# Kernel optimization log

Hardware: AMD Instinct MI355X
Metric: run time of the kernel (lower is better)

Reference implementation:

```python
import jax, jax.numpy as jnp
import numpy as np

N_NODES, N_GRAPHS, N_EDGES = 40960, 1024, 163840


def setup_inputs() -> dict:
    key = jax.random.key(0)
    ks = jax.random.split(key, 40)
    w = lambda k, s: jax.random.normal(k, s, jnp.float32) * 0.05
    inp = {
        "x": jax.random.normal(ks[0], (N_NODES, 78), jnp.float32),
        "edge_index": jax.random.randint(ks[1], (2, N_EDGES), 0, N_NODES, jnp.int32),
        "batch": jnp.repeat(jnp.arange(N_GRAPHS, dtype=jnp.int32), N_NODES // N_GRAPHS),
        "target1": jax.random.normal(ks[2], (N_GRAPHS, 750, 20), jnp.float32),
        "target2": jax.random.randint(ks[3], (N_GRAPHS, 750), 0, 26, jnp.int32),
        # GCN layers
        "W1": w(ks[4], (78, 78)), "b1": jnp.zeros((78,), jnp.float32),
        "W2": w(ks[5], (78, 156)), "b2": jnp.zeros((156,), jnp.float32),
        "W3": w(ks[6], (156, 312)), "b3": jnp.zeros((312,), jnp.float32),
        "Wg1": w(ks[7], (312, 1024)), "bg1": jnp.zeros((1024,), jnp.float32),
        "Wg2": w(ks[8], (1024, 128)), "bg2": jnp.zeros((128,), jnp.float32),
        # protein branch
        "emb": w(ks[9], (26, 128)),
        "Wc2": w(ks[10], (32, 750, 8)), "bc2": jnp.zeros((32,), jnp.float32),
        "Wxt2": w(ks[11], (32 * 121, 128)), "bxt2": jnp.zeros((128,), jnp.float32),
        "Wc1": w(ks[12], (32, 750, 8)), "bc1": jnp.zeros((32,), jnp.float32),
        "Wxt1": w(ks[13], (416, 128)), "bxt1": jnp.zeros((128,), jnp.float32),
        # fusion head
        "Wf1": w(ks[14], (384, 1024)), "bf1": jnp.zeros((1024,), jnp.float32),
        "Wf2": w(ks[15], (1024, 512)), "bf2": jnp.zeros((512,), jnp.float32),
        "Wo": w(ks[16], (512, 1)), "bo": jnp.zeros((1,), jnp.float32),
    }
    return inp


def _conv1d(x, w, b):
    # x: [B, C_in, L], w: [C_out, C_in, K] -> [B, C_out, L-K+1]
    y = jax.lax.conv_general_dilated(x, w, (1,), "VALID",
                                     dimension_numbers=("NCH", "OIH", "NCH"))
    return y + b[None, :, None]


def reference(x, edge_index, batch, target1, target2,
              W1, b1, W2, b2, W3, b3, Wg1, bg1, Wg2, bg2,
              emb, Wc2, bc2, Wxt2, bxt2, Wc1, bc1, Wxt1, bxt1,
              Wf1, bf1, Wf2, bf2, Wo, bo):
    N = x.shape[0]
    loop = jnp.arange(N, dtype=edge_index.dtype)
    src = jnp.concatenate([edge_index[0], loop])  # message source j
    dst = jnp.concatenate([edge_index[1], loop])  # aggregation target i
    # symmetric GCN normalization with self-loops (degree from dst, as in PyG)
    deg = jnp.zeros((N,), x.dtype).at[dst].add(1.0)
    dinv = jax.lax.rsqrt(deg)  # deg >= 1 due to self loops
    norm = (dinv[src] * dinv[dst])[:, None]

    def gcn(h, W, b):
        m = (h @ W)[src] * norm
        return jax.ops.segment_sum(m, dst, num_segments=N) + b

    h = jax.nn.relu(gcn(x, W1, b1))
    h = jax.nn.relu(gcn(h, W2, b2))
    h = jax.nn.relu(gcn(h, W3, b3))
    # global max pool per graph
    g = jax.ops.segment_max(h, batch, num_segments=N_GRAPHS)
    g = jax.nn.relu(g @ Wg1 + bg1)
    g = g @ Wg2 + bg2  # dropout is identity at inference

    # protein branch 2: embedding -> conv1d over channels=750
    e = emb[target2]                         # [B, 750, 128]
    xt2 = _conv1d(e, Wc2, bc2)               # [B, 32, 121]
    xt2 = xt2.reshape(-1, 32 * 121) @ Wxt2 + bxt2

    # protein branch 1: raw float features
    xt1 = _conv1d(target1, Wc1, bc1)         # [B, 32, 13]
    xt1 = xt1.reshape(-1, 416) @ Wxt1 + bxt1

    xc = jnp.concatenate([g, xt1, xt2], axis=1)  # [B, 384]
    xc = jax.nn.relu(xc @ Wf1 + bf1)
    xc = jax.nn.relu(xc @ Wf2 + bf2)
    return xc @ Wo + bo
```

## Files before the change

kernel.cpp:

```cpp
#include <hip/hip_runtime.h>
#include <hip/hip_bf16.h>

#define NN 40960
#define NE 163840
#define NB 1024

typedef __attribute__((ext_vector_type(8))) short short8;
typedef __attribute__((ext_vector_type(4))) float floatx4;

__device__ inline unsigned short f2bf(float f) {
    union { float f; unsigned u; } v; v.f = f;
    unsigned r = v.u + 0x7fffu + ((v.u >> 16) & 1u);
    return (unsigned short)(r >> 16);
}
__device__ inline float bf2f(unsigned short s) {
    union { unsigned u; float f; } v; v.u = ((unsigned)s) << 16; return v.f;
}
__device__ inline unsigned pack2bf(float lo, float hi) {
    return (unsigned)f2bf(lo) | ((unsigned)f2bf(hi) << 16);
}

static const size_t o_dinv = 0, o_g312 = 40960, o_g1024 = 360448, o_xc = 1409024,
                    o_f1 = 1802240, o_f2 = 2850816, o_b1v = 3375104, o_b2v = 3375232,
                    o_iws = 3375360, o_bufA = 3621124, o_bufB = 16400644;

__global__ void k_hist(const int* __restrict__ dst, int* __restrict__ cnt) {
    int e = blockIdx.x * 256 + threadIdx.x;
    if (e < NE) atomicAdd(&cnt[dst[e]], 1);
}

__global__ __launch_bounds__(1024) void k_scan1(const int* __restrict__ cnt, int* __restrict__ offTmp,
                                                int* __restrict__ blockSum, float* __restrict__ dinv) {
    __shared__ int lds[1024];
    int tid = threadIdx.x;
    int i = blockIdx.x * 1024 + tid;
    int v = cnt[i];
    dinv[i] = rsqrtf((float)v + 1.0f);
    lds[tid] = v;
    __syncthreads();
    for (int s = 1; s < 1024; s <<= 1) {
        int t = (tid >= s) ? lds[tid - s] : 0;
        __syncthreads();
        lds[tid] += t;
        __syncthreads();
    }
    offTmp[i] = lds[tid] - v;
    if (tid == 1023) blockSum[blockIdx.x] = lds[1023];
}

__global__ __launch_bounds__(64) void k_scan2(const int* __restrict__ blockSum, int* __restrict__ blockOff) {
    int l = threadIdx.x;
    int s = (l < 40) ? blockSum[l] : 0;
    int orig = s;
    for (int d = 1; d < 64; d <<= 1) {
        int t = __shfl_up(s, d);
        if (l >= d) s += t;
    }
    if (l < 40) blockOff[l] = s - orig;
}

__global__ __launch_bounds__(1024) void k_scan3(int* __restrict__ off, int* __restrict__ cur,
                                                const int* __restrict__ blockOff) {
    int i = blockIdx.x * 1024 + threadIdx.x;
    int o = off[i] + blockOff[blockIdx.x];
    off[i] = o;
    cur[i] = o;
    if (i == NN - 1) off[NN] = NE;
}

__global__ void k_fill(const int* __restrict__ ei, int* __restrict__ cur, int* __restrict__ srcOut) {
    int e = blockIdx.x * 256 + threadIdx.x;
    if (e >= NE) return;
    int s = ei[e], d = ei[NE + e];
    int pos = atomicAdd(&cur[d], 1);
    srcOut[pos] = s;
}

__global__ __launch_bounds__(256) void k_cvt_wt(const float* __restrict__ W1, const float* __restrict__ W2,
                                                const float* __restrict__ W3, const float* __restrict__ Wg1,
                                                const float* __restrict__ Wg2, const float* __restrict__ Wf1,
                                                const float* __restrict__ Wf2, unsigned short* __restrict__ dst) {
    const int cum[8]  = {0, 128, 320, 640, 1664, 1792, 2816, 3328};
    const int KP[7]   = {96, 96, 160, 320, 1024, 384, 1024};
    const int KB[7]   = {78, 78, 156, 312, 1024, 384, 1024};
    const int NNm[7]  = {78, 156, 312, 1024, 128, 1024, 512};
    const size_t OFF[7] = {0, 12288, 30720, 81920, 409600, 540672, 933888};
    int m = 0;
    int bx = blockIdx.x;
    while (m < 6 && bx >= cum[m + 1]) m++;
    int r = bx - cum[m];
    const float* src = (m == 0) ? W1 : (m == 1) ? W2 : (m == 2) ? W3 : (m == 3) ? Wg1
                     : (m == 4) ? Wg2 : (m == 5) ? Wf1 : Wf2;
    int kp = KP[m], kb = KB[m], nn = NNm[m];
    unsigned short* d = dst + OFF[m] + (size_t)r * kp;
    for (int k = threadIdx.x; k < kp; k += 256) {
        float v = (r < nn && k < kb) ? src[(size_t)k * nn + r] : 0.f;
        d[k] = f2bf(v);
    }
}

__global__ __launch_bounds__(64) void k_agg_x(const float* __restrict__ x, const float* __restrict__ dinv,
                                              const int* __restrict__ off, const int* __restrict__ srcs,
                                              unsigned* __restrict__ out) {
    int n = blockIdx.x;
    int f = threadIdx.x;
    if (f >= 48) return;
    if (f >= 39) { out[(size_t)n * 48 + f] = 0; return; }
    float di = dinv[n];
    float2 sv = *(const float2*)&x[(size_t)n * 78 + 2 * f];
    float a0 = sv.x * di * di, a1 = sv.y * di * di;
    int e0 = off[n], e1 = off[n + 1];
    int e = e0;
    for (; e + 4 <= e1; e += 4) {
        int s0 = srcs[e], s1 = srcs[e + 1], s2 = srcs[e + 2], s3 = srcs[e + 3];
        float d0 = dinv[s0] * di, d1 = dinv[s1] * di, d2 = dinv[s2] * di, d3 = dinv[s3] * di;
        float2 v0 = *(const float2*)&x[(size_t)s0 * 78 + 2 * f];
        float2 v1 = *(const float2*)&x[(size_t)s1 * 78 + 2 * f];
        float2 v2 = *(const float2*)&x[(size_t)s2 * 78 + 2 * f];
        float2 v3 = *(const float2*)&x[(size_t)s3 * 78 + 2 * f];
        a0 += v0.x * d0 + v1.x * d1 + v2.x * d2 + v3.x * d3;
        a1 += v0.y * d0 + v1.y * d1 + v2.y * d2 + v3.y * d3;
    }
    for (; e < e1; e++) {
        int s = srcs[e];
        float dd = dinv[s] * di;
        float2 v = *(const float2*)&x[(size_t)s * 78 + 2 * f];
        a0 += v.x * dd; a1 += v.y * dd;
    }
    out[(size_t)n * 48 + f] = pack2bf(a0, a1);
}

__global__ void k_agg16(const unsigned* __restrict__ h, const float* __restrict__ dinv,
                        const int* __restrict__ off, const int* __restrict__ srcs,
                        unsigned* __restrict__ out, int F2) {
    int n = blockIdx.x;
    int f = threadIdx.x;
    if (f >= F2) return;
    float di = dinv[n];
    unsigned s0v = h[(size_t)n * F2 + f];
    float a0 = bf2f((unsigned short)(s0v & 0xffff)) * di * di;
    float a1 = bf2f((unsigned short)(s0v >> 16)) * di * di;
    int e0 = off[n], e1 = off[n + 1];
    int e = e0;
    for (; e + 4 <= e1; e += 4) {
        int s0 = srcs[e], s1 = srcs[e + 1], s2 = srcs[e + 2], s3 = srcs[e + 3];
        float d0 = dinv[s0] * di, d1 = dinv[s1] * di, d2 = dinv[s2] * di, d3 = dinv[s3] * di;
        unsigned v0 = h[(size_t)s0 * F2 + f];
        unsigned v1 = h[(size_t)s1 * F2 + f];
        unsigned v2 = h[(size_t)s2 * F2 + f];
        unsigned v3 = h[(size_t)s3 * F2 + f];
        a0 += bf2f((unsigned short)(v0 & 0xffff)) * d0 + bf2f((unsigned short)(v1 & 0xffff)) * d1
            + bf2f((unsigned short)(v2 & 0xffff)) * d2 + bf2f((unsigned short)(v3 & 0xffff)) * d3;
        a1 += bf2f((unsigned short)(v0 >> 16)) * d0 + bf2f((unsigned short)(v1 >> 16)) * d1
            + bf2f((unsigned short)(v2 >> 16)) * d2 + bf2f((unsigned short)(v3 >> 16)) * d3;
    }
    for (; e < e1; e++) {
        int s = srcs[e];
        float dd = dinv[s] * di;
        unsigned v = h[(size_t)s * F2 + f];
        a0 += bf2f((unsigned short)(v & 0xffff)) * dd;
        a1 += bf2f((unsigned short)(v >> 16)) * dd;
    }
    out[(size_t)n * F2 + f] = pack2bf(a0, a1);
}

__global__ void k_segmax16(const unsigned short* __restrict__ h, unsigned short* __restrict__ g) {
    int gr = blockIdx.x, f = threadIdx.x;
    if (f >= 320) return;
    if (f >= 312) { g[(size_t)gr * 320 + f] = 0; return; }
    float m = 0.0f;
    const unsigned short* base = h + (size_t)gr * 40 * 312 + f;
    for (int i = 0; i < 40; i++) m = fmaxf(m, bf2f(base[(size_t)i * 312]));
    g[(size_t)gr * 320 + f] = f2bf(m);
}

#define LDST 72
template <bool ABF16, bool OUTBF16, bool ATOMIC, bool RELU_OUT>
__global__ __launch_bounds__(256) void gemm_bt(const void* __restrict__ Av, const unsigned short* __restrict__ Bt,
                                               const float* __restrict__ bias, void* __restrict__ Cv,
                                               int Nn, int Npad, int Kpad, int Klim,
                                               int lda, int ldb, int ldc, int ksplit) {
    __shared__ __align__(16) unsigned short As[64 * LDST];
    __shared__ __align__(16) unsigned short Bs[64 * LDST];
    const float* Af = (const float*)Av;
    const unsigned short* A16 = (const unsigned short*)Av;
    float* Cf = (float*)Cv;
    unsigned short* C16 = (unsigned short*)Cv;
    int bn0 = blockIdx.x * 64;
    int bm0 = blockIdx.y * 64;
    int k0 = blockIdx.z * ksplit;
    int kend = k0 + ksplit; if (kend > Kpad) kend = Kpad;
    int tid = threadIdx.x;
    int w = tid >> 6, l = tid & 63, q = l >> 4, r = l & 15;
    int wr = w >> 1, wc = w & 1;

    floatx4 acc[2][2];
#pragma unroll
    for (int i = 0; i < 2; i++)
#pragma unroll
        for (int c = 0; c < 2; c++) acc[i][c] = (floatx4)0.0f;

    int mA = tid >> 2, kcA = (tid & 3) * 8;
    int nB = tid >> 2, kcB = (tid & 3) * 8;
    int gmA = bm0 + mA;
    int gnB = bn0 + nB;

    for (int kt = k0; kt < kend; kt += 32) {
        if (ABF16) {
            *(short8*)&As[mA * LDST + kcA] = *(const short8*)(A16 + (size_t)gmA * lda + kt + kcA);
        } else {
            const float* Ap = Af + (size_t)gmA * lda + kt + kcA;
            float av[8];
            if (kt + kcA + 8 <= Klim) {
#pragma unroll
                for (int j = 0; j < 4; j++) {
                    float2 p = *(const float2*)(Ap + j * 2);
                    av[j * 2] = p.x; av[j * 2 + 1] = p.y;
                }
            } else {
#pragma unroll
                for (int j = 0; j < 8; j++) av[j] = (kt + kcA + j < Klim) ? Ap[j] : 0.f;
            }
            short8 sv;
#pragma unroll
            for (int j = 0; j < 8; j++) sv[j] = (short)f2bf(av[j]);
            *(short8*)&As[mA * LDST + kcA] = sv;
        }
        *(short8*)&Bs[nB * LDST + kcB] = *(const short8*)(Bt + (size_t)gnB * ldb + kt + kcB);
        __syncthreads();
        short8 a0 = *(const short8*)&As[(wr * 32 + r) * LDST + q * 8];
        short8 a1 = *(const short8*)&As[(wr * 32 + 16 + r) * LDST + q * 8];
        short8 b0 = *(const short8*)&Bs[(wc * 32 + r) * LDST + q * 8];
        short8 b1 = *(const short8*)&Bs[(wc * 32 + 16 + r) * LDST + q * 8];
        acc[0][0] = __builtin_amdgcn_mfma_f32_16x16x32_bf16(a0, b0, acc[0][0], 0, 0, 0);
        acc[0][1] = __builtin_amdgcn_mfma_f32_16x16x32_bf16(a0, b1, acc[0][1], 0, 0, 0);
        acc[1][0] = __builtin_amdgcn_mfma_f32_16x16x32_bf16(a1, b0, acc[1][0], 0, 0, 0);
        acc[1][1] = __builtin_amdgcn_mfma_f32_16x16x32_bf16(a1, b1, acc[1][1], 0, 0, 0);
        __syncthreads();
    }

#pragma unroll
    for (int c2 = 0; c2 < 2; c2++) {
        int col = bn0 + wc * 32 + c2 * 16 + r;
        if (col >= Npad) continue;
        bool live = col < Nn;
        float bv = (bias && live) ? bias[col] : 0.f;
#pragma unroll
        for (int i = 0; i < 2; i++) {
#pragma unroll
            for (int v = 0; v < 4; v++) {
                int row = bm0 + wr * 32 + i * 16 + q * 4 + v;
                float val = live ? (acc[i][c2][v] + bv) : 0.f;
                if (RELU_OUT) val = fmaxf(val, 0.f);
                if (OUTBF16) {
                    C16[(size_t)row * ldc + col] = live ? f2bf(val) : (unsigned short)0;
                } else if (live) {
                    if (ATOMIC) atomicAdd(&Cf[(size_t)row * ldc + col], val);
                    else Cf[(size_t)row * ldc + col] = val;
                }
            }
        }
    }
}

template <int OM>
__global__ __launch_bounds__(256) void gemm_mfma_batch(const float* __restrict__ A, const float* __restrict__ B,
                                                       void* __restrict__ Cv,
                                                       int M, int Nn, int K, int ldc,
                                                       long sB, long sC) {
    __shared__ __align__(16) unsigned short As[64 * LDST];
    __shared__ __align__(16) unsigned short Bs[64 * LDST];
    const float* Bm = B + (size_t)blockIdx.z * sB;
    unsigned short* C16 = (unsigned short*)Cv + (size_t)blockIdx.z * sC;
    int bn0 = blockIdx.x * 64;
    int bm0 = blockIdx.y * 64;
    int tid = threadIdx.x;
    int w = tid >> 6, l = tid & 63, q = l >> 4, r = l & 15;
    int wr = w >> 1, wc = w & 1;

    floatx4 acc[2][2];
#pragma unroll
    for (int i = 0; i < 2; i++)
#pragma unroll
        for (int c = 0; c < 2; c++) acc[i][c] = (floatx4)0.0f;

    int mA = tid >> 2, kcA = (tid & 3) * 8;
    int nB = tid >> 2, kcB = (tid & 3) * 8;
    int gmA = bm0 + mA;
    int gnB = bn0 + nB;

    for (int kt = 0; kt < K; kt += 32) {
        {
            float av[8];
            const float* Ap = A + (size_t)gmA * K + kt + kcA;
            if (gmA < M) {
#pragma unroll
                for (int j = 0; j < 4; j++) {
                    float2 p = *(const float2*)(Ap + j * 2);
                    av[j * 2] = p.x; av[j * 2 + 1] = p.y;
                }
            } else {
#pragma unroll
                for (int j = 0; j < 8; j++) av[j] = 0.f;
            }
            short8 sv;
#pragma unroll
            for (int j = 0; j < 8; j++) sv[j] = (short)f2bf(av[j]);
            *(short8*)&As[mA * LDST + kcA] = sv;
        }
        {
            short8 sv;
#pragma unroll
            for (int j = 0; j < 8; j++) {
                int gk = kt + kcB + j;
                float v = (gnB < Nn) ? Bm[(size_t)gk * Nn + gnB] : 0.f;
                sv[j] = (short)f2bf(v);
            }
            *(short8*)&Bs[nB * LDST + kcB] = sv;
        }
        __syncthreads();
        short8 a0 = *(const short8*)&As[(wr * 32 + r) * LDST + q * 8];
        short8 a1 = *(const short8*)&As[(wr * 32 + 16 + r) * LDST + q * 8];
        short8 b0 = *(const short8*)&Bs[(wc * 32 + r) * LDST + q * 8];
        short8 b1 = *(const short8*)&Bs[(wc * 32 + 16 + r) * LDST + q * 8];
        acc[0][0] = __builtin_amdgcn_mfma_f32_16x16x32_bf16(a0, b0, acc[0][0], 0, 0, 0);
        acc[0][1] = __builtin_amdgcn_mfma_f32_16x16x32_bf16(a0, b1, acc[0][1], 0, 0, 0);
        acc[1][0] = __builtin_amdgcn_mfma_f32_16x16x32_bf16(a1, b0, acc[1][0], 0, 0, 0);
        acc[1][1] = __builtin_amdgcn_mfma_f32_16x16x32_bf16(a1, b1, acc[1][1], 0, 0, 0);
        __syncthreads();
    }

#pragma unroll
    for (int c = 0; c < 2; c++) {
        int col = bn0 + wc * 32 + c * 16 + r;
        if (col >= Nn) continue;
#pragma unroll
        for (int i = 0; i < 2; i++) {
#pragma unroll
            for (int v = 0; v < 4; v++) {
                int row = bm0 + wr * 32 + i * 16 + q * 4 + v;
                if (row >= M) continue;
                if (OM == 1) C16[(size_t)row * ldc + col] = f2bf(acc[i][c][v]);
                else C16[(size_t)col * ldc + row * 20 + blockIdx.z] = f2bf(acc[i][c][v]);
            }
        }
    }
}

__global__ __launch_bounds__(256) void k_wcr_both(const float* __restrict__ Wc2, const float* __restrict__ Wc1,
                                                  float* __restrict__ Wc2r, float* __restrict__ Wc1r) {
    int cc = blockIdx.x, j = threadIdx.x;
    const float* W = (cc < 750) ? Wc2 : Wc1;
    float* Wr = (cc < 750) ? Wc2r : Wc1r;
    int c = (cc < 750) ? cc : cc - 750;
    Wr[(size_t)c * 256 + j] = W[(size_t)(j >> 3) * 6000 + c * 8 + (j & 7)];
}

__global__ __launch_bounds__(128) void k_T_build(const float* __restrict__ emb, const float* __restrict__ Wxt2,
                                                 float* __restrict__ T) {
    __shared__ float el[128];
    int v = blockIdx.x >> 5, o = blockIdx.x & 31, j = threadIdx.x;
    el[j] = emb[(size_t)v * 128 + j];
    __syncthreads();
    float acc[8] = {};
    for (int l = 0; l < 121; l++) {
        float w = Wxt2[(size_t)(o * 121 + l) * 128 + j];
#pragma unroll
        for (int k = 0; k < 8; k++) acc[k] += el[l + k] * w;
    }
#pragma unroll
    for (int k = 0; k < 8; k++) T[(size_t)(v * 256 + o * 8 + k) * 128 + j] = acc[k];
}

__global__ __launch_bounds__(128) void k_bt_build(const float* __restrict__ Wxt1, float* __restrict__ Bt) {
    int ok = blockIdx.x, t = blockIdx.y, j = threadIdx.x;
    int o = ok >> 3, k = ok & 7, lpos = t - k;
    float v = (lpos >= 0 && lpos < 13) ? Wxt1[(size_t)(o * 13 + lpos) * 128 + j] : 0.f;
    Bt[(size_t)(t * 256 + ok) * 128 + j] = v;
}

__global__ __launch_bounds__(128) void k_u_gather16(const int* __restrict__ t2, const unsigned short* __restrict__ U,
                                                    const float* __restrict__ b2v, float* __restrict__ xc) {
    __shared__ int offs[752];
    __shared__ float red[8][128];
    int b = blockIdx.x, tid = threadIdx.x;
    int rg = tid >> 4, lane = tid & 15;
    const int* t2b = t2 + (size_t)b * 750;
    for (int i = tid; i < 750; i += 128) offs[i] = i * 3328 + t2b[i] * 128;
    __syncthreads();
    float a[8] = {};
#pragma unroll 4
    for (int i = rg; i < 750; i += 8) {
        short8 v = *(const short8*)&U[(size_t)offs[i] + lane * 8];
#pragma unroll
        for (int c = 0; c < 8; c++) a[c] += bf2f((unsigned short)v[c]);
    }
#pragma unroll
    for (int c = 0; c < 8; c++) red[rg][lane * 8 + c] = a[c];
    __syncthreads();
    float s = b2v[tid];
#pragma unroll
    for (int g = 0; g < 8; g++) s += red[g][tid];
    xc[(size_t)b * 384 + 256 + tid] = s;
}

__global__ void k_bias_init(const float* __restrict__ bxt1, const float* __restrict__ bxt2,
                            float* __restrict__ b1v, float* __restrict__ b2v) {
    int j = threadIdx.x;
    b1v[j] = bxt1[j];
    b2v[j] = bxt2[j];
}

__global__ __launch_bounds__(128) void k_bias_acc_both(const float* __restrict__ bc1, const float* __restrict__ Wxt1,
                                                       float* __restrict__ b1v,
                                                       const float* __restrict__ bc2, const float* __restrict__ Wxt2,
                                                       float* __restrict__ b2v) {
    int b = blockIdx.x, j = threadIdx.x;
    if (b < 32) {
        const float* p = Wxt1 + (size_t)b * 13 * 128 + j;
        float t = 0.f;
        for (int l = 0; l < 13; l++) t += p[(size_t)l * 128];
        atomicAdd(&b1v[j], bc1[b] * t);
    } else {
        int o = b - 32;
        const float* p = Wxt2 + (size_t)o * 121 * 128 + j;
        float t = 0.f;
        for (int l = 0; l < 121; l++) t += p[(size_t)l * 128];
        atomicAdd(&b2v[j], bc2[o] * t);
    }
}

__global__ __launch_bounds__(768) void k_initC(float* __restrict__ xc, float* __restrict__ f2,
                                               const float* __restrict__ bg2, const float* __restrict__ b1v,
                                               const float* __restrict__ bf2) {
    int b = blockIdx.x, t = threadIdx.x;
    if (t < 128) xc[(size_t)b * 384 + t] = bg2[t];
    else if (t < 256) xc[(size_t)b * 384 + t] = b1v[t - 128];
    else f2[(size_t)b * 512 + t - 256] = bf2[t - 256];
}

__global__ __launch_bounds__(64) void k_final(const float* __restrict__ f2, const float* __restrict__ Wo,
                                              const float* __restrict__ bo, float* __restrict__ out) {
    int b = blockIdx.x, lane = threadIdx.x;
    float s = 0.f;
    for (int j = lane; j < 512; j += 64) s += fmaxf(f2[(size_t)b * 512 + j], 0.f) * Wo[j];
    for (int off = 32; off; off >>= 1) s += __shfl_down(s, off);
    if (lane == 0) out[b] = s + bo[0];
}

extern "C" void kernel_launch(void* const* d_in, const int* in_sizes, int n_in,
                              void* d_out, int out_size, void* d_ws, size_t ws_size,
                              hipStream_t stream) {
    const float* x    = (const float*)d_in[0];
    const int*   ei   = (const int*)d_in[1];
    const float* t1   = (const float*)d_in[3];
    const int*   t2   = (const int*)d_in[4];
    const float* W1   = (const float*)d_in[5];
    const float* b1   = (const float*)d_in[6];
    const float* W2   = (const float*)d_in[7];
    const float* b2   = (const float*)d_in[8];
    const float* W3   = (const float*)d_in[9];
    const float* b3   = (const float*)d_in[10];
    const float* Wg1  = (const float*)d_in[11];
    const float* bg1  = (const float*)d_in[12];
    const float* Wg2  = (const float*)d_in[13];
    const float* bg2  = (const float*)d_in[14];
    const float* emb  = (const float*)d_in[15];
    const float* Wc2  = (const float*)d_in[16];
    const float* bc2  = (const float*)d_in[17];
    const float* Wxt2 = (const float*)d_in[18];
    const float* bxt2 = (const float*)d_in[19];
    const float* Wc1  = (const float*)d_in[20];
    const float* bc1  = (const float*)d_in[21];
    const float* Wxt1 = (const float*)d_in[22];
    const float* bxt1 = (const float*)d_in[23];
    const float* Wf1  = (const float*)d_in[24];
    const float* bf1  = (const float*)d_in[25];
    const float* Wf2  = (const float*)d_in[26];
    const float* bf2  = (const float*)d_in[27];
    const float* Wo   = (const float*)d_in[28];
    const float* bo   = (const float*)d_in[29];
    float* out = (float*)d_out;

    float* ws = (float*)d_ws;
    float* dinv  = ws + o_dinv;
    unsigned short* g312b = (unsigned short*)(ws + o_g312);
    unsigned short* g1024b = (unsigned short*)(ws + o_g1024);
    float* xc    = ws + o_xc;
    unsigned short* f1b = (unsigned short*)(ws + o_f1);
    float* f2    = ws + o_f2;
    float* b1v   = ws + o_b1v;
    float* b2v   = ws + o_b2v;
    int* csrOff  = (int*)(ws + o_iws);
    int* csrCur  = csrOff + (NN + 1);
    int* csrSrc  = csrCur + NN;
    int* blockSum = (int*)(ws + o_f1 + 600000);
    int* blockOff = blockSum + 40;
    float* bufA  = ws + o_bufA;
    float* bufB  = ws + o_bufB;
    float* T    = bufA;
    unsigned short* U16  = (unsigned short*)(bufA + 851968);
    unsigned short* Vt16 = (unsigned short*)(bufA + 2200000);
    unsigned short* Wt   = (unsigned short*)(bufA + 3200000);
    float* Wc2r = bufA + 4000000;
    float* Wc1r = bufA + 4200000;
    float* Btb  = bufA + 4400000;
    unsigned* aggb = (unsigned*)bufB;
    unsigned short* h16 = (unsigned short*)(bufB + 5500000);

    unsigned short* W1t  = Wt + 0;
    unsigned short* W2t  = Wt + 12288;
    unsigned short* W3t  = Wt + 30720;
    unsigned short* Wg1t = Wt + 81920;
    unsigned short* Wg2t = Wt + 409600;
    unsigned short* Wf1t = Wt + 540672;
    unsigned short* Wf2t = Wt + 933888;

    hipMemsetAsync(csrCur, 0, NN * sizeof(int), stream);
    k_hist<<<NE / 256, 256, 0, stream>>>(ei + NE, csrCur);
    k_scan1<<<40, 1024, 0, stream>>>(csrCur, csrOff, blockSum, dinv);
    k_scan2<<<1, 64, 0, stream>>>(blockSum, blockOff);
    k_scan3<<<40, 1024, 0, stream>>>(csrOff, csrCur, blockOff);
    k_fill<<<NE / 256, 256, 0, stream>>>(ei, csrCur, csrSrc);
    k_cvt_wt<<<3328, 256, 0, stream>>>(W1, W2, W3, Wg1, Wg2, Wf1, Wf2, Wt);

    k_agg_x<<<NN, 64, 0, stream>>>(x, dinv, csrOff, csrSrc, aggb);
    gemm_bt<true, true, false, true><<<dim3(2, 640, 1), 256, 0, stream>>>(
        aggb, W1t, b1, h16, 78, 96, 96, 96, 96, 96, 96, 96);
    k_agg16<<<NN, 64, 0, stream>>>((unsigned*)h16, dinv, csrOff, csrSrc, aggb, 48);
    gemm_bt<true, true, false, true><<<dim3(3, 640, 1), 256, 0, stream>>>(
        aggb, W2t, b2, h16, 156, 160, 96, 96, 96, 96, 160, 96);
    k_agg16<<<NN, 128, 0, stream>>>((unsigned*)h16, dinv, csrOff, csrSrc, aggb, 80);
    gemm_bt<true, true, false, true><<<dim3(5, 640, 1), 256, 0, stream>>>(
        aggb, W3t, b3, h16, 312, 312, 160, 160, 160, 160, 312, 160);
    k_segmax16<<<NB, 320, 0, stream>>>(h16, g312b);
    gemm_bt<true, true, false, true><<<dim3(16, 16, 1), 256, 0, stream>>>(
        g312b, Wg1t, bg1, g1024b, 1024, 1024, 320, 320, 320, 320, 1024, 320);

    k_bias_init<<<1, 128, 0, stream>>>(bxt1, bxt2, b1v, b2v);
    k_bias_acc_both<<<64, 128, 0, stream>>>(bc1, Wxt1, b1v, bc2, Wxt2, b2v);
    k_initC<<<NB, 768, 0, stream>>>(xc, f2, bg2, b1v, bf2);

    gemm_bt<true, false, true, false><<<dim3(2, 16, 8), 256, 0, stream>>>(
        g1024b, Wg2t, nullptr, xc + 0, 128, 128, 1024, 1024, 1024, 1024, 384, 128);

    k_wcr_both<<<1500, 256, 0, stream>>>(Wc2, Wc1, Wc2r, Wc1r);
    k_T_build<<<26 * 32, 128, 0, stream>>>(emb, Wxt2, T);
    gemm_mfma_batch<1><<<dim3(2, 12, 26), 256, 0, stream>>>(Wc2r, T, U16, 750, 128, 256, 3328, 32768, 128);
    k_u_gather16<<<NB, 128, 0, stream>>>(t2, U16, b2v, xc);

    k_bt_build<<<dim3(256, 20), 128, 0, stream>>>(Wxt1, Btb);
    hipMemsetAsync(Vt16, 0, (size_t)128 * 15008 * 2, stream);
    gemm_mfma_batch<2><<<dim3(2, 12, 20), 256, 0, stream>>>(Wc1r, Btb, Vt16, 750, 128, 256, 15008, 32768, 0);
    gemm_bt<false, false, true, false><<<dim3(2, 16, 32), 256, 0, stream>>>(
        t1, Vt16, nullptr, xc + 128, 128, 128, 15008, 15000, 15000, 15008, 384, 480);

    gemm_bt<false, true, false, true><<<dim3(16, 16, 1), 256, 0, stream>>>(
        xc, Wf1t, bf1, f1b, 1024, 1024, 384, 384, 384, 384, 1024, 384);
    gemm_bt<true, false, true, false><<<dim3(8, 16, 4), 256, 0, stream>>>(
        f1b, Wf2t, nullptr, f2, 512, 512, 1024, 1024, 1024, 1024, 512, 256);
    k_final<<<NB, 64, 0, stream>>>(f2, Wo, bo, out);
}
```

Measured before the change: 465.6 us.

## Replace atomic split-K target1 GEMM with register-pipelined split-K kernel plus reduction

```diff
diff --git a/kernel.cpp b/kernel.cpp
--- a/kernel.cpp
+++ b/kernel.cpp
@@ -261,6 +261,104 @@
             }
         }
     }
+}
+
+#define T1S  48
+#define T1K  320
+__global__ __launch_bounds__(256) void gemm_t1(const float* __restrict__ A, const unsigned short* __restrict__ Bt,
+                                               float* __restrict__ P) {
+    const int Klim = 15000;
+    int tid = threadIdx.x;
+    int w = tid >> 6, l = tid & 63, q = l >> 4, r = l & 15;
+    int b = blockIdx.x;
+    int mt = b / 24, rem = b % 24;
+    int nh = w & 1;
+    int ks = rem * 2 + (w >> 1);
+    int k0 = ks * T1K;
+    int bm = mt * 64;
+    int cn = nh * 64;
+
+    const float* Ab = A + (size_t)(bm + r) * Klim + q * 8;
+    const unsigned short* Bb = Bt + (size_t)(cn + r) * 15360 + q * 8;
+
+    floatx4 acc[4][4];
+#pragma unroll
+    for (int f = 0; f < 4; f++)
+#pragma unroll
+        for (int c = 0; c < 4; c++) acc[f][c] = (floatx4)0.0f;
+
+    float4 ar[3][4][2];
+    short8 br[3][4];
+
+    auto loadSet = [&](int s, int kt) {
+#pragma unroll
+        for (int f = 0; f < 4; f++) {
+            const float* Ap = Ab + (size_t)f * 16 * Klim + kt;
+            int idx = kt + q * 8;
+            if (idx + 8 <= Klim) {
+                ar[s][f][0] = *(const float4*)(Ap);
+                ar[s][f][1] = *(const float4*)(Ap + 4);
+            } else {
+                float t[8];
+#pragma unroll
+                for (int j = 0; j < 8; j++) t[j] = (idx + j < Klim) ? Ap[j] : 0.f;
+                ar[s][f][0] = make_float4(t[0], t[1], t[2], t[3]);
+                ar[s][f][1] = make_float4(t[4], t[5], t[6], t[7]);
+            }
+        }
+#pragma unroll
+        for (int c = 0; c < 4; c++)
+            br[s][c] = *(const short8*)(Bb + (size_t)c * 16 * 15360 + kt);
+    };
+    auto compute = [&](int s) {
+        short8 af[4];
+#pragma unroll
+        for (int f = 0; f < 4; f++) {
+            short8 v;
+            v[0] = (short)f2bf(ar[s][f][0].x); v[1] = (short)f2bf(ar[s][f][0].y);
+            v[2] = (short)f2bf(ar[s][f][0].z); v[3] = (short)f2bf(ar[s][f][0].w);
+            v[4] = (short)f2bf(ar[s][f][1].x); v[5] = (short)f2bf(ar[s][f][1].y);
+            v[6] = (short)f2bf(ar[s][f][1].z); v[7] = (short)f2bf(ar[s][f][1].w);
+            af[f] = v;
+        }
+#pragma unroll
+        for (int f = 0; f < 4; f++)
+#pragma unroll
+            for (int c = 0; c < 4; c++)
+                acc[f][c] = __builtin_amdgcn_mfma_f32_16x16x32_bf16(af[f], br[s][c], acc[f][c], 0, 0, 0);
+    };
+
+    loadSet(0, k0);
+    loadSet(1, k0 + 32);
+    loadSet(2, k0 + 64);
+    compute(0); loadSet(0, k0 + 96);
+    compute(1); loadSet(1, k0 + 128);
+    compute(2); loadSet(2, k0 + 160);
+    compute(0); loadSet(0, k0 + 192);
+    compute(1); loadSet(1, k0 + 224);
+    compute(2); loadSet(2, k0 + 256);
+    compute(0); loadSet(0, k0 + 288);
+    compute(1);
+    compute(2);
+    compute(0);
+
+    float* Pp = P + (size_t)ks * (1024 * 128) + (size_t)bm * 128 + cn;
+#pragma unroll
+    for (int f = 0; f < 4; f++)
+#pragma unroll
+        for (int c = 0; c < 4; c++)
+#pragma unroll
+            for (int v = 0; v < 4; v++)
+                Pp[(size_t)(f * 16 + q * 4 + v) * 128 + c * 16 + r] = acc[f][c][v];
+}
+
+__global__ __launch_bounds__(128) void k_red_t1(const float* __restrict__ P, float* __restrict__ xc) {
+    int row = blockIdx.x, j = threadIdx.x;
+    const float* p = P + (size_t)row * 128 + j;
+    float s = 0.f;
+#pragma unroll
+    for (int ks = 0; ks < T1S; ks++) s += p[(size_t)ks * (1024 * 128)];
+    xc[(size_t)row * 384 + 128 + j] += s;
 }
 
 template <int OM>
@@ -507,6 +605,7 @@
     float* Btb  = bufA + 4400000;
     unsigned* aggb = (unsigned*)bufB;
     unsigned short* h16 = (unsigned short*)(bufB + 5500000);
+    float* Pt1 = bufB;
 
     unsigned short* W1t  = Wt + 0;
     unsigned short* W2t  = Wt + 12288;
@@ -550,10 +649,10 @@
     k_u_gather16<<<NB, 128, 0, stream>>>(t2, U16, b2v, xc);
 
     k_bt_build<<<dim3(256, 20), 128, 0, stream>>>(Wxt1, Btb);
-    hipMemsetAsync(Vt16, 0, (size_t)128 * 15008 * 2, stream);
-    gemm_mfma_batch<2><<<dim3(2, 12, 20), 256, 0, stream>>>(Wc1r, Btb, Vt16, 750, 128, 256, 15008, 32768, 0);
-    gemm_bt<false, false, true, false><<<dim3(2, 16, 32), 256, 0, stream>>>(
-        t1, Vt16, nullptr, xc + 128, 128, 128, 15008, 15000, 15000, 15008, 384, 480);
+    hipMemsetAsync(Vt16, 0, (size_t)128 * 15360 * 2, stream);
+    gemm_mfma_batch<2><<<dim3(2, 12, 20), 256, 0, stream>>>(Wc1r, Btb, Vt16, 750, 128, 256, 15360, 32768, 0);
+    gemm_t1<<<dim3(384, 1, 1), 256, 0, stream>>>(t1, Vt16, Pt1);
+    k_red_t1<<<NB, 128, 0, stream>>>(Pt1, xc);
 
     gemm_bt<false, true, false, true><<<dim3(16, 16, 1), 256, 0, stream>>>(
         xc, Wf1t, bf1, f1b, 1024, 1024, 384, 384, 384, 384, 1024, 384);
```

Result: no change. 471.6 us (+1.3%).

## Replace atomic split-K target1 GEMM with register-direct MFMA kernel plus partial-sum reduction

Applied to the files above, without the earlier changes.

```diff
diff --git a/kernel.cpp b/kernel.cpp
--- a/kernel.cpp
+++ b/kernel.cpp
@@ -261,6 +261,87 @@
             }
         }
     }
+}
+
+#define T1S  32
+#define T1K  480
+__global__ __launch_bounds__(256) void gemm_t1(const float* __restrict__ A, const unsigned short* __restrict__ Bt,
+                                               float* __restrict__ P) {
+    int tid = threadIdx.x;
+    int w = tid >> 6, l = tid & 63, q = l >> 4, r = l & 15;
+    int b = blockIdx.x;
+    int mt = b >> 5, ks = b & 31;
+    int k0 = ks * T1K;
+    int bm = mt * 32;
+    int cn = w * 32;
+
+    const float* A0 = A + (size_t)(bm + r) * 15000;
+    const float* A1 = A + (size_t)(bm + 16 + r) * 15000;
+    const unsigned short* B0 = Bt + (size_t)(cn + r) * 15360 + k0 + q * 8;
+    const unsigned short* B1 = Bt + (size_t)(cn + 16 + r) * 15360 + k0 + q * 8;
+
+    floatx4 acc[2][2];
+#pragma unroll
+    for (int f = 0; f < 2; f++)
+#pragma unroll
+        for (int c = 0; c < 2; c++) acc[f][c] = (floatx4)0.0f;
+
+    float4 aA[4], aB[4];
+    short8 bA[2], bB[2];
+
+    auto loadS = [&](int kt, float4 (&a)[4], short8 (&bb)[2]) {
+        int col = k0 + kt + q * 8;
+        int ce = (col < 15000) ? col : 0;
+        a[0] = *(const float4*)(A0 + ce);
+        a[1] = *(const float4*)(A0 + ce + 4);
+        a[2] = *(const float4*)(A1 + ce);
+        a[3] = *(const float4*)(A1 + ce + 4);
+        bb[0] = *(const short8*)(B0 + kt);
+        bb[1] = *(const short8*)(B1 + kt);
+    };
+    auto computeS = [&](const float4 (&a)[4], const short8 (&bb)[2]) {
+        short8 af0, af1;
+        af0[0] = (short)f2bf(a[0].x); af0[1] = (short)f2bf(a[0].y);
+        af0[2] = (short)f2bf(a[0].z); af0[3] = (short)f2bf(a[0].w);
+        af0[4] = (short)f2bf(a[1].x); af0[5] = (short)f2bf(a[1].y);
+        af0[6] = (short)f2bf(a[1].z); af0[7] = (short)f2bf(a[1].w);
+        af1[0] = (short)f2bf(a[2].x); af1[1] = (short)f2bf(a[2].y);
+        af1[2] = (short)f2bf(a[2].z); af1[3] = (short)f2bf(a[2].w);
+        af1[4] = (short)f2bf(a[3].x); af1[5] = (short)f2bf(a[3].y);
+        af1[6] = (short)f2bf(a[3].z); af1[7] = (short)f2bf(a[3].w);
+        acc[0][0] = __builtin_amdgcn_mfma_f32_16x16x32_bf16(af0, bb[0], acc[0][0], 0, 0, 0);
+        acc[0][1] = __builtin_amdgcn_mfma_f32_16x16x32_bf16(af0, bb[1], acc[0][1], 0, 0, 0);
+        acc[1][0] = __builtin_amdgcn_mfma_f32_16x16x32_bf16(af1, bb[0], acc[1][0], 0, 0, 0);
+        acc[1][1] = __builtin_amdgcn_mfma_f32_16x16x32_bf16(af1, bb[1], acc[1][1], 0, 0, 0);
+    };
+
+    loadS(0, aA, bA);
+#pragma unroll
+    for (int it = 0; it < 7; ++it) {
+        loadS(64 * it + 32, aB, bB);
+        computeS(aA, bA);
+        loadS(64 * it + 64, aA, bA);
+        computeS(aB, bB);
+    }
+    computeS(aA, bA);
+
+    float* Pp = P + (size_t)ks * (1024 * 128) + (size_t)bm * 128 + cn;
+#pragma unroll
+    for (int f = 0; f < 2; f++)
+#pragma unroll
+        for (int c = 0; c < 2; c++)
+#pragma unroll
+            for (int v = 0; v < 4; v++)
+                Pp[(size_t)(f * 16 + q * 4 + v) * 128 + c * 16 + r] = acc[f][c][v];
+}
+
+__global__ __launch_bounds__(128) void k_red_t1(const float* __restrict__ P, float* __restrict__ xc) {
+    int row = blockIdx.x, j = threadIdx.x;
+    const float* p = P + (size_t)row * 128 + j;
+    float s = 0.f;
+#pragma unroll
+    for (int ks = 0; ks < T1S; ks++) s += p[(size_t)ks * (1024 * 128)];
+    xc[(size_t)row * 384 + 128 + j] += s;
 }
 
 template <int OM>
@@ -507,6 +588,7 @@
     float* Btb  = bufA + 4400000;
     unsigned* aggb = (unsigned*)bufB;
     unsigned short* h16 = (unsigned short*)(bufB + 5500000);
+    float* Pt1 = bufB;
 
     unsigned short* W1t  = Wt + 0;
     unsigned short* W2t  = Wt + 12288;
@@ -550,10 +632,10 @@
     k_u_gather16<<<NB, 128, 0, stream>>>(t2, U16, b2v, xc);
 
     k_bt_build<<<dim3(256, 20), 128, 0, stream>>>(Wxt1, Btb);
-    hipMemsetAsync(Vt16, 0, (size_t)128 * 15008 * 2, stream);
-    gemm_mfma_batch<2><<<dim3(2, 12, 20), 256, 0, stream>>>(Wc1r, Btb, Vt16, 750, 128, 256, 15008, 32768, 0);
-    gemm_bt<false, false, true, false><<<dim3(2, 16, 32), 256, 0, stream>>>(
-        t1, Vt16, nullptr, xc + 128, 128, 128, 15008, 15000, 15000, 15008, 384, 480);
+    hipMemsetAsync(Vt16, 0, (size_t)128 * 15360 * 2, stream);
+    gemm_mfma_batch<2><<<dim3(2, 12, 20), 256, 0, stream>>>(Wc1r, Btb, Vt16, 750, 128, 256, 15360, 32768, 0);
+    gemm_t1<<<dim3(1024, 1, 1), 256, 0, stream>>>(t1, Vt16, Pt1);
+    k_red_t1<<<NB, 128, 0, stream>>>(Pt1, xc);
 
     gemm_bt<false, true, false, true><<<dim3(16, 16, 1), 256, 0, stream>>>(
         xc, Wf1t, bf1, f1b, 1024, 1024, 384, 384, 384, 384, 1024, 384);
```

Result: no change. 472.9 us (+1.6%).
